# Kernel optimization log

Measured on AMD Instinct MI355X. Metric: run time of the kernel, lower is better.

## Reference

```python
import jax, jax.numpy as jnp
import numpy as np

B, C, H, W = 2, 192, 48, 512
EMB, HEADS, DOUT, MAXM, THR, EPS = 64, 2, 192, 64, 0.01, 1e-5
DV = DOUT // HEADS  # per-head value dim (96)


def setup_inputs() -> dict:
    key = jax.random.key(0)
    ks = jax.random.split(key, 16)
    s = 0.02
    inp = {
        "l": jax.random.normal(ks[0], (B, C, H, W), jnp.float32),
        "r": jax.random.normal(ks[1], (B, C, H, W), jnp.float32),
        "ln_l_g": jnp.ones((C,), jnp.float32),
        "ln_l_b": jnp.zeros((C,), jnp.float32),
        "ln_r_g": jnp.ones((C,), jnp.float32),
        "ln_r_b": jnp.zeros((C,), jnp.float32),
    }
    ki = 2
    for p in ("rtl", "ltr"):
        inp[p + "_wq"] = jax.random.normal(ks[ki], (HEADS * EMB, C, 3), jnp.float32) * s; ki += 1
        inp[p + "_bq"] = jnp.zeros((HEADS * EMB,), jnp.float32)
        inp[p + "_wk"] = jax.random.normal(ks[ki], (HEADS * EMB, C, 3), jnp.float32) * s; ki += 1
        inp[p + "_bk"] = jnp.zeros((HEADS * EMB,), jnp.float32)
        inp[p + "_wv"] = jax.random.normal(ks[ki], (DOUT, C, 3), jnp.float32) * s; ki += 1
        inp[p + "_bv"] = jnp.zeros((DOUT,), jnp.float32)
        inp[p + "_wo"] = jax.random.normal(ks[ki], (DOUT, DOUT), jnp.float32) * s; ki += 1
        inp[p + "_bo"] = jnp.zeros((DOUT,), jnp.float32)
    inp["ffl_w"] = jax.random.normal(ks[ki], (DOUT, DOUT), jnp.float32) * s; ki += 1
    inp["ffl_b"] = jnp.zeros((DOUT,), jnp.float32)
    inp["ffr_w"] = jax.random.normal(ks[ki], (DOUT, DOUT), jnp.float32) * s; ki += 1
    inp["ffr_b"] = jnp.zeros((DOUT,), jnp.float32)
    return inp


def _layernorm(x, g, b):
    m = x.mean(-1, keepdims=True)
    v = x.var(-1, keepdims=True)
    return (x - m) / jnp.sqrt(v + EPS) * g + b


def _conv1d(x, w, b):
    # x: [N, Cin, L], w: [Cout, Cin, 3], same padding
    y = jax.lax.conv_general_dilated(x, w, (1,), [(1, 1)], dimension_numbers=("NCH", "OIH", "NCH"))
    return y + b[None, :, None]


def _conv_attn(q_seq, k_seq, v_seq, wq, bq, wk, bk, wv, bv, wo, bo, mask):
    # q_seq/k_seq/v_seq: [N, L, C]; mask: [L, L] bool (True = masked)
    N, L, _ = q_seq.shape
    Q = _conv1d(q_seq.transpose(0, 2, 1), wq, bq).reshape(N, HEADS, EMB, L).transpose(0, 1, 3, 2)  # b h l d
    K = _conv1d(k_seq.transpose(0, 2, 1), wk, bk).reshape(N, HEADS, EMB, L).transpose(0, 1, 3, 2)
    V = _conv1d(v_seq.transpose(0, 2, 1), wv, bv).reshape(N, HEADS, DV, L).transpose(0, 1, 3, 2)
    A = jnp.einsum("bhqd,bhkd->bhqk", Q, K) / np.sqrt(EMB).astype(np.float32)
    A = jnp.where(mask, -jnp.inf, A)
    A = jax.nn.softmax(A, axis=-1)
    A = A * (A > THR)  # valid_mask thresholding after softmax
    O = jnp.einsum("bhqk,bhkd->bhqd", A, V)
    O = O.transpose(0, 2, 1, 3).reshape(N, L, DOUT)
    return jnp.einsum("nld,od->nlo", O, wo) + bo, A


def reference(l, r, ln_l_g, ln_l_b, ln_r_g, ln_r_b,
              rtl_wq, rtl_bq, rtl_wk, rtl_bk, rtl_wv, rtl_bv, rtl_wo, rtl_bo,
              ltr_wq, ltr_bq, ltr_wk, ltr_bk, ltr_wv, ltr_bv, ltr_wo, ltr_bo,
              ffl_w, ffl_b, ffr_w, ffr_b):
    ls = l.transpose(0, 2, 3, 1).reshape(B * H, W, C)  # (b h) w c
    rs = r.transpose(0, 2, 3, 1).reshape(B * H, W, C)
    ln_ = _layernorm(ls, ln_l_g, ln_l_b)
    rn_ = _layernorm(rs, ln_r_g, ln_r_b)
    i = jnp.arange(W)[:, None]
    j = jnp.arange(W)[None, :]
    mask_left = (j < i) | (j - i > MAXM)   # left query i attends keys j in [i, i+MAXM]
    mask_right = (j > i) | (i - j > MAXM)  # right query i attends keys j in [i-MAXM, i]
    l_mha, A_rtl = _conv_attn(ln_, rn_, rs, rtl_wq, rtl_bq, rtl_wk, rtl_bk, rtl_wv, rtl_bv, rtl_wo, rtl_bo, mask_left)
    r_mha, A_ltr = _conv_attn(rn_, ln_, ls, ltr_wq, ltr_bq, ltr_wk, ltr_bk, ltr_wv, ltr_bv, ltr_wo, ltr_bo, mask_right)
    lo = ls + l_mha
    ro = rs + r_mha
    lo = lo + (jnp.einsum("nwc,oc->nwo", lo, ffl_w) + ffl_b)
    ro = ro + (jnp.einsum("nwc,oc->nwo", ro, ffr_w) + ffr_b)
    l_out = lo.reshape(B, H, W, C).transpose(0, 3, 1, 2)
    r_out = ro.reshape(B, H, W, C).transpose(0, 3, 1, 2)
    return (l_out, r_out, A_rtl, A_ltr)
```

## Files before the change

### kernel.cpp

```cpp
#include <hip/hip_runtime.h>
#include <cstddef>
#include <cstdint>

constexpr int kC = 192;
constexpr int kW = 512;
constexpr int kHH = 48;

typedef unsigned short u16;
typedef __attribute__((ext_vector_type(8))) short bf16x8;
typedef __attribute__((ext_vector_type(4))) float f32x4;
typedef __attribute__((ext_vector_type(4))) unsigned short us4;

__device__ inline u16 f2bf(float f) {
  union { float f; uint32_t u; } v; v.f = f;
  uint32_t r = v.u + 0x7FFF + ((v.u >> 16) & 1);
  return (u16)(r >> 16);
}
__device__ inline float bf2f(u16 u) {
  return __uint_as_float(((uint32_t)u) << 16);
}

__global__ void __launch_bounds__(256) prep_kernel(
    const float* __restrict__ xl, const float* __restrict__ xr,
    const float* __restrict__ gl, const float* __restrict__ bl,
    const float* __restrict__ gr, const float* __restrict__ br,
    u16* __restrict__ lnl, u16* __restrict__ lraw,
    u16* __restrict__ lnr, u16* __restrict__ rraw,
    const float* wq0, const float* wk0, const float* wv0,
    const float* wq1, const float* wk1, const float* wv1,
    const float* bq0, const float* bk0, const float* bv0,
    const float* bq1, const float* bk1, const float* bv1,
    const float* wo0, const float* wo1, const float* fw0, const float* fw1,
    u16* __restrict__ wall, u16* __restrict__ pfw, float* __restrict__ ball) {
  int bid = blockIdx.x;
  int tid = threadIdx.x;
  if (bid >= 1536) {
    int idx = (bid - 1536) * 256 + tid;
    if (idx < 516096) {
      int dir = idx / 258048, off = idx % 258048;
      const float* src; int soff;
      if (off < 73728) { src = dir ? wq1 : wq0; soff = off; }
      else if (off < 147456) { src = dir ? wk1 : wk0; soff = off - 73728; }
      else { src = dir ? wv1 : wv0; soff = off - 147456; }
      int o = soff / 576, k = soff % 576, t = k / 192, c = k % 192;
      wall[idx] = f2bf(src[((size_t)o * kC + c) * 3 + t]);
    } else if (idx < 516096 + 147456) {
      int i2 = idx - 516096;
      int mat = i2 / 36864, off = i2 % 36864;
      const float* src = mat == 0 ? wo0 : mat == 1 ? wo1 : mat == 2 ? fw0 : fw1;
      pfw[i2] = f2bf(src[off]);
    } else if (idx < 516096 + 147456 + 896) {
      int bi = idx - 516096 - 147456;
      int dir = bi / 448, boff = bi % 448;
      const float* s; int so;
      if (boff < 128) { s = dir ? bq1 : bq0; so = boff; }
      else if (boff < 256) { s = dir ? bk1 : bk0; so = boff - 128; }
      else { s = dir ? bv1 : bv0; so = boff - 256; }
      ball[bi] = s[so];
    }
    return;
  }
  int w0 = (bid & 7) * 64;
  int n = (bid >> 3) % 96;
  int side = bid / 768;
  const float* x = side ? xr : xl;
  const float* g = side ? gr : gl;
  const float* b = side ? br : bl;
  u16* lnout = side ? lnr : lnl;
  u16* rawout = side ? rraw : lraw;
  int bb = n / kHH, h = n % kHH;
  __shared__ float tile[64][193];
  __shared__ float red[8][64];
  __shared__ float mean_s[64], rstd_s[64];
  int lane = tid & 63, wv = tid >> 6;
  for (int c = wv; c < kC; c += 4)
    tile[lane][c] = x[(((size_t)bb * kC + c) * kHH + h) * kW + w0 + lane];
  __syncthreads();
  {
    int w = tid & 63, part = tid >> 6;
    float s = 0.f, s2 = 0.f;
    const float* row = &tile[w][0];
    for (int c = part * 48; c < part * 48 + 48; ++c) {
      float v = row[c];
      s += v; s2 += v * v;
    }
    red[part][w] = s;
    red[part + 4][w] = s2;
  }
  __syncthreads();
  if (tid < 64) {
    float s = red[0][tid] + red[1][tid] + red[2][tid] + red[3][tid];
    float s2 = red[4][tid] + red[5][tid] + red[6][tid] + red[7][tid];
    float m = s * (1.f / 192.f);
    float var = s2 * (1.f / 192.f) - m * m;
    mean_s[tid] = m;
    rstd_s[tid] = rsqrtf(var + 1e-5f);
  }
  __syncthreads();
  for (int u = tid; u < 64 * 48; u += 256) {
    int w = u / 48, c4 = (u % 48) * 4;
    float mm = mean_s[w], rs = rstd_s[w];
    us4 lp, rp;
#pragma unroll
    for (int j = 0; j < 4; ++j) {
      float raw = tile[w][c4 + j];
      rp[j] = f2bf(raw);
      lp[j] = f2bf((raw - mm) * rs * g[c4 + j] + b[c4 + j]);
    }
    size_t idx = ((size_t)n * kW + w0 + w) * kC + c4;
    *reinterpret_cast<us4*>(&lnout[idx]) = lp;
    *reinterpret_cast<us4*>(&rawout[idx]) = rp;
  }
}

template <int NF>
__device__ __forceinline__ void conv_core(
    const u16* __restrict__ in, const u16* __restrict__ w2,
    int n, int l0, u16* As, f32x4 (&acc)[4][NF]) {
  int tid = threadIdx.x;
  int wid = tid >> 6, lane = tid & 63;
  int wm = wid >> 1, wn = wid & 1;
  int lr = lane & 15, g = lane >> 4;
  for (int u = tid; u < 130 * 48; u += 256) {
    int row = u / 48, q = u % 48;
    int l = l0 - 1 + row;
    us4 v = {0, 0, 0, 0};
    if (l >= 0 && l < kW)
      v = *reinterpret_cast<const us4*>(in + ((size_t)n * kW + l) * kC + q * 4);
    *reinterpret_cast<us4*>(&As[row * 200 + q * 4]) = v;
  }
  __syncthreads();
  const u16* wbase = w2 + (size_t)(wn * NF * 16 + lr) * 576 + g * 8;
#pragma unroll
  for (int t = 0; t < 3; ++t) {
#pragma unroll
    for (int c0 = 0; c0 < 192; c0 += 64) {
#pragma unroll
      for (int ks = 0; ks < 2; ++ks) {
        bf16x8 a[4], b[NF];
#pragma unroll
        for (int mf = 0; mf < 4; ++mf)
          a[mf] = *reinterpret_cast<const bf16x8*>(
              &As[(wm * 64 + mf * 16 + lr + t) * 200 + c0 + ks * 32 + g * 8]);
#pragma unroll
        for (int nf = 0; nf < NF; ++nf)
          b[nf] = *reinterpret_cast<const bf16x8*>(
              wbase + (size_t)nf * 16 * 576 + t * 192 + c0 + ks * 32);
#pragma unroll
        for (int mf = 0; mf < 4; ++mf)
#pragma unroll
          for (int nf = 0; nf < NF; ++nf)
            acc[mf][nf] = __builtin_amdgcn_mfma_f32_16x16x32_bf16(a[mf], b[nf], acc[mf][nf], 0, 0, 0);
      }
    }
  }
}

__global__ void __launch_bounds__(256) conv_qk(
    const u16* __restrict__ lnl, const u16* __restrict__ lnr,
    const u16* __restrict__ wall, const float* __restrict__ ball,
    u16* __restrict__ Qbf, u16* __restrict__ Kbf, float* __restrict__ A0) {
  if (blockIdx.y == 4) {
    int fid = blockIdx.z * 4 + blockIdx.x;
    int base_row = fid * 256;
    f32x4 z4 = {0.f, 0.f, 0.f, 0.f};
    for (int u = threadIdx.x; u < 256 * 128; u += 256) {
      int lrow = u >> 7, c4 = u & 127;
      int rg = base_row + lrow;
      int nh = rg >> 9, i = rg & 511;
      int q0 = i & ~63;
      int w1 = q0 + 128 > 512 ? 512 : q0 + 128;
      int col = c4 * 4;
      if (col < q0 || col >= w1)
        __builtin_nontemporal_store(z4, reinterpret_cast<f32x4*>(
            A0 + (size_t)nh * 262144 + (size_t)i * 512 + col));
    }
    return;
  }
  int l0 = blockIdx.x * 128;
  int jid = blockIdx.y;
  int n = blockIdx.z;
  int dir = jid >> 1, which = jid & 1;
  const u16* in = which == 0 ? (dir ? lnr : lnl) : (dir ? lnl : lnr);
  const u16* w2 = wall + (size_t)dir * 258048 + which * 73728;
  const float* bias = ball + dir * 448 + which * 128;

  __shared__ __attribute__((aligned(16))) u16 As[130 * 200];
  f32x4 acc[4][4] = {};
  conv_core<4>(in, w2, n, l0, As, acc);

  int tid = threadIdx.x;
  int wid = tid >> 6, lane = tid & 63;
  int wm = wid >> 1, wn = wid & 1;
  int lr = lane & 15, g = lane >> 4;
  __syncthreads();
  u16* Ts = As;
#pragma unroll
  for (int nf = 0; nf < 4; ++nf) {
    int o = wn * 64 + nf * 16 + lr;
    float bsv = bias[o];
#pragma unroll
    for (int mf = 0; mf < 4; ++mf) {
      int lbase = wm * 64 + mf * 16 + g * 4;
#pragma unroll
      for (int rg = 0; rg < 4; ++rg)
        Ts[(lbase + rg) * 132 + o] = f2bf(acc[mf][nf][rg] + bsv);
    }
  }
  __syncthreads();
  u16* outp = (which == 0 ? Qbf : Kbf) + (size_t)dir * 6291456;
  for (int u = tid; u < 4096; u += 256) {
    int hh = u >> 11;
    int rem = u & 2047;
    int l = rem >> 4, q4 = (rem & 15) * 4;
    us4 v = *reinterpret_cast<const us4*>(&Ts[l * 132 + hh * 64 + q4]);
    *reinterpret_cast<us4*>(
        &outp[((size_t)(n * 2 + hh) * kW + l0 + l) * 64 + q4]) = v;
  }
}

__global__ void __launch_bounds__(256) conv_v(
    const u16* __restrict__ lraw, const u16* __restrict__ rraw,
    const u16* __restrict__ wall, const float* __restrict__ ball,
    u16* __restrict__ Vbf, float* __restrict__ A1) {
  if (blockIdx.y == 2) {
    int fid = blockIdx.z * 4 + blockIdx.x;
    int base_row = fid * 256;
    f32x4 z4 = {0.f, 0.f, 0.f, 0.f};
    for (int u = threadIdx.x; u < 256 * 128; u += 256) {
      int lrow = u >> 7, c4 = u & 127;
      int rg = base_row + lrow;
      int nh = rg >> 9, i = rg & 511;
      int q0 = i & ~63;
      int w0 = q0 >= 64 ? q0 - 64 : 0;
      int col = c4 * 4;
      if (col < w0 || col >= q0 + 64)
        __builtin_nontemporal_store(z4, reinterpret_cast<f32x4*>(
            A1 + (size_t)nh * 262144 + (size_t)i * 512 + col));
    }
    return;
  }
  int l0 = blockIdx.x * 128;
  int dir = blockIdx.y;
  int n = blockIdx.z;
  const u16* in = dir ? lraw : rraw;
  const u16* w2 = wall + (size_t)dir * 258048 + 147456;
  const float* bias = ball + dir * 448 + 256;

  __shared__ __attribute__((aligned(16))) u16 As[130 * 200];
  f32x4 acc[4][6] = {};
  conv_core<6>(in, w2, n, l0, As, acc);

  int tid = threadIdx.x;
  int wid = tid >> 6, lane = tid & 63;
  int wm = wid >> 1, wn = wid & 1;
  int lr = lane & 15, g = lane >> 4;
  u16* outp = Vbf + (size_t)dir * 9437184;
#pragma unroll
  for (int nf = 0; nf < 6; ++nf) {
    int e = nf * 16 + lr;
    float bsv = bias[wn * 96 + e];
#pragma unroll
    for (int mf = 0; mf < 4; ++mf) {
      int lb = l0 + wm * 64 + mf * 16 + g * 4;
      us4 p;
#pragma unroll
      for (int rg = 0; rg < 4; ++rg) p[rg] = f2bf(acc[mf][nf][rg] + bsv);
      *reinterpret_cast<us4*>(&outp[((size_t)(n * 2 + wn) * 96 + e) * kW + lb]) = p;
    }
  }
}

__global__ void __launch_bounds__(256) attn_mfma(
    const u16* __restrict__ Qbf, const u16* __restrict__ Kbf,
    const u16* __restrict__ Vbf, float* __restrict__ Abase,
    u16* __restrict__ Obf) {
  int qb = blockIdx.x;
  int nh = blockIdx.y;
  int dir = blockIdx.z;
  int q0 = qb * 64;
  int k_start = dir == 0 ? q0 : (q0 >= 64 ? q0 - 64 : 0);
  int k_end = dir == 0 ? (q0 + 128 <= kW ? q0 + 128 : kW) : q0 + 64;
  int kfr = (k_end - k_start) >> 4;
  const u16* Q = Qbf + ((size_t)dir * 192 + nh) * kW * 64;
  const u16* K = Kbf + ((size_t)dir * 192 + nh) * kW * 64;
  const u16* V = Vbf + ((size_t)dir * 192 + nh) * 96 * kW;
  float* Aout = Abase + (size_t)dir * 50331648 + (size_t)nh * kW * kW;
  u16* Obase = Obf + (size_t)dir * 9437184;

  __shared__ __attribute__((aligned(16))) u16 smem[22272];
  u16* Ks = smem;
  u16* Ps = smem;
  u16* Vt = smem + 9216;

  int tid = threadIdx.x;
  int wid = tid >> 6, lane = tid & 63;
  int lr = lane & 15, g = lane >> 4;

  for (int u = tid; u < 128 * 16; u += 256) {
    int row = u >> 4, c4 = (u & 15) * 4;
    *reinterpret_cast<us4*>(&Ks[row * 72 + c4]) =
        *reinterpret_cast<const us4*>(&K[(size_t)(k_start + row) * 64 + c4]);
  }
  for (int u = tid; u < 96 * 32; u += 256) {
    int row = u >> 5, c4 = (u & 31) * 4;
    *reinterpret_cast<us4*>(&Vt[row * 136 + c4]) =
        *reinterpret_cast<const us4*>(&V[(size_t)row * kW + k_start + c4]);
  }
  const u16* Qrow = Q + (size_t)(q0 + wid * 16 + lr) * 64 + g * 8;
  bf16x8 bq0 = *reinterpret_cast<const bf16x8*>(Qrow);
  bf16x8 bq1 = *reinterpret_cast<const bf16x8*>(Qrow + 32);
  __syncthreads();

  int lo_k = q0 + wid * 16 - (dir == 0 ? 0 : 64) - k_start;
  int hi_k = q0 + wid * 16 + 15 + (dir == 0 ? 64 : 0) - k_start;

  f32x4 sT[8];
#pragma unroll
  for (int kf = 0; kf < 8; ++kf) sT[kf] = f32x4{0.f, 0.f, 0.f, 0.f};
#pragma unroll
  for (int kf = 0; kf < 8; ++kf) {
    if (kf * 16 + 15 >= lo_k && kf * 16 <= hi_k) {
      bf16x8 ak0 = *reinterpret_cast<const bf16x8*>(&Ks[(kf * 16 + lr) * 72 + g * 8]);
      sT[kf] = __builtin_amdgcn_mfma_f32_16x16x32_bf16(ak0, bq0, sT[kf], 0, 0, 0);
      bf16x8 ak1 = *reinterpret_cast<const bf16x8*>(&Ks[(kf * 16 + lr) * 72 + 32 + g * 8]);
      sT[kf] = __builtin_amdgcn_mfma_f32_16x16x32_bf16(ak1, bq1, sT[kf], 0, 0, 0);
    }
  }

  int i = q0 + wid * 16 + lr;
  float mx = -INFINITY;
#pragma unroll
  for (int kf = 0; kf < 8; ++kf) {
#pragma unroll
    for (int r = 0; r < 4; ++r) {
      int jj = k_start + kf * 16 + g * 4 + r;
      bool valid = (jj < k_end) &&
                   (dir == 0 ? (jj >= i && jj - i <= 64) : (jj <= i && i - jj <= 64));
      float v = valid ? sT[kf][r] * 0.125f : -INFINITY;
      sT[kf][r] = v;
      mx = fmaxf(mx, v);
    }
  }
  mx = fmaxf(mx, __shfl_xor(mx, 16));
  mx = fmaxf(mx, __shfl_xor(mx, 32));
  float ssum = 0.f;
#pragma unroll
  for (int kf = 0; kf < 8; ++kf) {
#pragma unroll
    for (int r = 0; r < 4; ++r) {
      float e = __expf(sT[kf][r] - mx);
      sT[kf][r] = e;
      ssum += e;
    }
  }
  ssum += __shfl_xor(ssum, 16);
  ssum += __shfl_xor(ssum, 32);
  float inv = 1.f / ssum;

  __syncthreads();

  {
    float* arow = Aout + (size_t)i * kW + k_start;
#pragma unroll
    for (int kf = 0; kf < 8; ++kf) {
      f32x4 pv;
      us4 pb;
#pragma unroll
      for (int r = 0; r < 4; ++r) {
        float p = sT[kf][r] * inv;
        p = (p > 0.01f) ? p : 0.f;
        pv[r] = p;
        pb[r] = f2bf(p);
      }
      *reinterpret_cast<us4*>(&Ps[(wid * 16 + lr) * 136 + kf * 16 + g * 4]) = pb;
      if (kf < kfr)
        __builtin_nontemporal_store(pv, reinterpret_cast<f32x4*>(arow + kf * 16 + g * 4));
    }
  }
  __syncthreads();

  f32x4 oacc[6];
#pragma unroll
  for (int ef = 0; ef < 6; ++ef) oacc[ef] = f32x4{0.f, 0.f, 0.f, 0.f};
#pragma unroll
  for (int kc = 0; kc < 4; ++kc) {
    if (kc * 32 + 31 >= lo_k && kc * 32 <= hi_k) {
      bf16x8 ap = *reinterpret_cast<const bf16x8*>(&Ps[(wid * 16 + lr) * 136 + kc * 32 + g * 8]);
#pragma unroll
      for (int ef = 0; ef < 6; ++ef) {
        bf16x8 bv = *reinterpret_cast<const bf16x8*>(&Vt[(ef * 16 + lr) * 136 + kc * 32 + g * 8]);
        oacc[ef] = __builtin_amdgcn_mfma_f32_16x16x32_bf16(ap, bv, oacc[ef], 0, 0, 0);
      }
    }
  }
  __syncthreads();
  u16* Os2 = smem;
#pragma unroll
  for (int ef = 0; ef < 6; ++ef) {
    int e = ef * 16 + lr;
#pragma unroll
    for (int r = 0; r < 4; ++r)
      Os2[(wid * 16 + g * 4 + r) * 104 + e] = f2bf(oacc[ef][r]);
  }
  __syncthreads();
  int n_ = nh >> 1, h_ = nh & 1;
  for (int u = tid; u < 64 * 24; u += 256) {
    int q = u / 24, c4 = (u % 24) * 4;
    *reinterpret_cast<us4*>(&Obase[((size_t)n_ * kW + q0 + q) * kC + h_ * 96 + c4]) =
        *reinterpret_cast<const us4*>(&Os2[q * 104 + c4]);
  }
}

__global__ void __launch_bounds__(256) projff_mfma(
    const u16* __restrict__ pfw,
    const float* __restrict__ bo0, const float* __restrict__ bo1,
    const float* __restrict__ fb0, const float* __restrict__ fb1,
    const u16* __restrict__ Obf, const u16* __restrict__ lraw,
    const u16* __restrict__ rraw, float* __restrict__ outbase) {
  int l0 = blockIdx.x * 64;
  int z = blockIdx.y;
  int dir = z / 96, n = z % 96;
  const u16* wo2 = pfw + (dir ? 36864 : 0);
  const u16* fw2 = pfw + 73728 + (dir ? 36864 : 0);
  const float* bo_ = dir ? bo1 : bo0;
  const float* fb_ = dir ? fb1 : fb0;
  const u16* Osrc = Obf + (size_t)dir * 9437184;
  const u16* resbf = dir ? rraw : lraw;
  float* outb = outbase + (size_t)dir * 9437184;
  int bb = n / kHH, h = n % kHH;

  __shared__ __attribute__((aligned(16))) u16 Xs[64 * 200];
  __shared__ __attribute__((aligned(16))) u16 Rs[64 * 200];

  int tid = threadIdx.x;
  int wid = tid >> 6, lane = tid & 63;
  int wm = wid >> 1, wn = wid & 1;
  int lr = lane & 15, g = lane >> 4;

  for (int u = tid; u < 64 * 48; u += 256) {
    int row = u / 48, q = u % 48;
    size_t src = ((size_t)n * kW + l0 + row) * kC + q * 4;
    *reinterpret_cast<us4*>(&Xs[row * 200 + q * 4]) =
        *reinterpret_cast<const us4*>(&Osrc[src]);
    *reinterpret_cast<us4*>(&Rs[row * 200 + q * 4]) =
        *reinterpret_cast<const us4*>(&resbf[src]);
  }
  __syncthreads();

  const u16* wobase = wo2 + (size_t)(wn * 96 + lr) * kC + g * 8;
  const u16* fwbase = fw2 + (size_t)(wn * 96 + lr) * kC + g * 8;

  f32x4 accp[2][6] = {};
#pragma unroll
  for (int c0 = 0; c0 < 192; c0 += 64) {
#pragma unroll
    for (int ks = 0; ks < 2; ++ks) {
      bf16x8 a[2], b[6];
#pragma unroll
      for (int m2 = 0; m2 < 2; ++m2)
        a[m2] = *reinterpret_cast<const bf16x8*>(
            &Xs[(wm * 32 + m2 * 16 + lr) * 200 + c0 + ks * 32 + g * 8]);
#pragma unroll
      for (int nf = 0; nf < 6; ++nf)
        b[nf] = *reinterpret_cast<const bf16x8*>(
            wobase + (size_t)nf * 16 * kC + c0 + ks * 32);
#pragma unroll
      for (int m2 = 0; m2 < 2; ++m2)
#pragma unroll
        for (int nf = 0; nf < 6; ++nf)
          accp[m2][nf] = __builtin_amdgcn_mfma_f32_16x16x32_bf16(a[m2], b[nf], accp[m2][nf], 0, 0, 0);
    }
  }
  __syncthreads();
#pragma unroll
  for (int nf = 0; nf < 6; ++nf) {
    int o = wn * 96 + nf * 16 + lr;
    float bv = bo_[o];
#pragma unroll
    for (int m2 = 0; m2 < 2; ++m2) {
#pragma unroll
      for (int r = 0; r < 4; ++r) {
        int l = wm * 32 + m2 * 16 + g * 4 + r;
        float v = accp[m2][nf][r] + bv + bf2f(Rs[l * 200 + o]);
        accp[m2][nf][r] = v;
        Xs[l * 200 + o] = f2bf(v);
      }
    }
  }
  __syncthreads();

  f32x4 accf[2][6] = {};
#pragma unroll
  for (int c0 = 0; c0 < 192; c0 += 64) {
#pragma unroll
    for (int ks = 0; ks < 2; ++ks) {
      bf16x8 a[2], b[6];
#pragma unroll
      for (int m2 = 0; m2 < 2; ++m2)
        a[m2] = *reinterpret_cast<const bf16x8*>(
            &Xs[(wm * 32 + m2 * 16 + lr) * 200 + c0 + ks * 32 + g * 8]);
#pragma unroll
      for (int nf = 0; nf < 6; ++nf)
        b[nf] = *reinterpret_cast<const bf16x8*>(
            fwbase + (size_t)nf * 16 * kC + c0 + ks * 32);
#pragma unroll
      for (int m2 = 0; m2 < 2; ++m2)
#pragma unroll
        for (int nf = 0; nf < 6; ++nf)
          accf[m2][nf] = __builtin_amdgcn_mfma_f32_16x16x32_bf16(a[m2], b[nf], accf[m2][nf], 0, 0, 0);
    }
  }
#pragma unroll
  for (int nf = 0; nf < 6; ++nf) {
    int o = wn * 96 + nf * 16 + lr;
    float bv = fb_[o];
#pragma unroll
    for (int m2 = 0; m2 < 2; ++m2) {
      f32x4 ov;
#pragma unroll
      for (int r = 0; r < 4; ++r)
        ov[r] = accf[m2][nf][r] + bv + accp[m2][nf][r];
      int l = l0 + wm * 32 + m2 * 16 + g * 4;
      *reinterpret_cast<f32x4*>(&outb[(((size_t)bb * kC + o) * kHH + h) * kW + l]) = ov;
    }
  }
}

extern "C" void kernel_launch(void* const* d_in, const int* in_sizes, int n_in,
                              void* d_out, int out_size, void* d_ws, size_t ws_size,
                              hipStream_t stream) {
  const float* l = (const float*)d_in[0];
  const float* r = (const float*)d_in[1];
  float* out = (float*)d_out;
  float* ws = (float*)d_ws;

  u16* lnl_bf  = (u16*)(ws + 0);
  u16* lnr_bf  = (u16*)(ws + 4718592);
  u16* lraw_bf = (u16*)(ws + 9437184);
  u16* rraw_bf = (u16*)(ws + 14155776);
  u16* wall    = (u16*)(ws + 18874368);
  float* ball  = ws + 19136512;
  u16* Qbf     = (u16*)(ws + 19137536);
  u16* Kbf     = (u16*)(ws + 25428992);
  u16* Vbf     = (u16*)(ws + 31720448);
  u16* Obf     = (u16*)(ws + 41157632);
  u16* pfw     = (u16*)(ws + 50594816);

  float* A0 = out + (size_t)18874368;
  float* A1 = out + (size_t)69206016;

  int wp_items = 516096 + 147456 + 896;
  int wp_blocks = (wp_items + 255) / 256;
  prep_kernel<<<1536 + wp_blocks, 256, 0, stream>>>(
      l, r, (const float*)d_in[2], (const float*)d_in[3],
      (const float*)d_in[4], (const float*)d_in[5],
      lnl_bf, lraw_bf, lnr_bf, rraw_bf,
      (const float*)d_in[6], (const float*)d_in[8], (const float*)d_in[10],
      (const float*)d_in[14], (const float*)d_in[16], (const float*)d_in[18],
      (const float*)d_in[7], (const float*)d_in[9], (const float*)d_in[11],
      (const float*)d_in[15], (const float*)d_in[17], (const float*)d_in[19],
      (const float*)d_in[12], (const float*)d_in[20],
      (const float*)d_in[22], (const float*)d_in[24],
      wall, pfw, ball);

  conv_qk<<<dim3(4, 5, 96), 256, 0, stream>>>(
      lnl_bf, lnr_bf, wall, ball, Qbf, Kbf, A0);
  conv_v<<<dim3(4, 3, 96), 256, 0, stream>>>(
      lraw_bf, rraw_bf, wall, ball, Vbf, A1);

  attn_mfma<<<dim3(8, 192, 2), 256, 0, stream>>>(
      Qbf, Kbf, Vbf, A0, Obf);

  projff_mfma<<<dim3(8, 192), 256, 0, stream>>>(
      pfw, (const float*)d_in[13], (const float*)d_in[21],
      (const float*)d_in[23], (const float*)d_in[25],
      Obf, lraw_bf, rraw_bf, out);
}
```

Before: 355.9 us.

## Fuse attention with output projection and feed-forward into one kernel

Merges the attention kernel and the projection/FF kernel so each block computes both heads for a 64-row tile, keeps the concatenated head outputs in shared memory, and then applies the output projection, residual and FF in place. This removes the bf16 O round trip through global memory and one kernel launch. In exchange the grid halves, the heads are processed sequentially inside each block, and shared memory per block grows to about 70KB, which may lower occupancy.

```diff
diff --git a/kernel.cpp b/kernel.cpp
--- a/kernel.cpp
+++ b/kernel.cpp
@@ -271,183 +271,162 @@
   }
 }
 
-__global__ void __launch_bounds__(256) attn_mfma(
+__global__ void __launch_bounds__(256) attn_projff(
     const u16* __restrict__ Qbf, const u16* __restrict__ Kbf,
-    const u16* __restrict__ Vbf, float* __restrict__ Abase,
-    u16* __restrict__ Obf) {
+    const u16* __restrict__ Vbf, const u16* __restrict__ pfw,
+    const float* __restrict__ bo0, const float* __restrict__ bo1,
+    const float* __restrict__ fb0, const float* __restrict__ fb1,
+    const u16* __restrict__ lraw, const u16* __restrict__ rraw,
+    float* __restrict__ Abase, float* __restrict__ outbase) {
   int qb = blockIdx.x;
-  int nh = blockIdx.y;
+  int n = blockIdx.y;
   int dir = blockIdx.z;
   int q0 = qb * 64;
   int k_start = dir == 0 ? q0 : (q0 >= 64 ? q0 - 64 : 0);
   int k_end = dir == 0 ? (q0 + 128 <= kW ? q0 + 128 : kW) : q0 + 64;
   int kfr = (k_end - k_start) >> 4;
-  const u16* Q = Qbf + ((size_t)dir * 192 + nh) * kW * 64;
-  const u16* K = Kbf + ((size_t)dir * 192 + nh) * kW * 64;
-  const u16* V = Vbf + ((size_t)dir * 192 + nh) * 96 * kW;
-  float* Aout = Abase + (size_t)dir * 50331648 + (size_t)nh * kW * kW;
-  u16* Obase = Obf + (size_t)dir * 9437184;
-
-  __shared__ __attribute__((aligned(16))) u16 smem[22272];
+
+  __shared__ __attribute__((aligned(16))) u16 smem[35072];
   u16* Ks = smem;
   u16* Ps = smem;
   u16* Vt = smem + 9216;
+  u16* Rs = smem;
+  u16* Os = smem + 22272;
 
   int tid = threadIdx.x;
   int wid = tid >> 6, lane = tid & 63;
   int lr = lane & 15, g = lane >> 4;
 
-  for (int u = tid; u < 128 * 16; u += 256) {
-    int row = u >> 4, c4 = (u & 15) * 4;
-    *reinterpret_cast<us4*>(&Ks[row * 72 + c4]) =
-        *reinterpret_cast<const us4*>(&K[(size_t)(k_start + row) * 64 + c4]);
-  }
-  for (int u = tid; u < 96 * 32; u += 256) {
-    int row = u >> 5, c4 = (u & 31) * 4;
-    *reinterpret_cast<us4*>(&Vt[row * 136 + c4]) =
-        *reinterpret_cast<const us4*>(&V[(size_t)row * kW + k_start + c4]);
-  }
-  const u16* Qrow = Q + (size_t)(q0 + wid * 16 + lr) * 64 + g * 8;
-  bf16x8 bq0 = *reinterpret_cast<const bf16x8*>(Qrow);
-  bf16x8 bq1 = *reinterpret_cast<const bf16x8*>(Qrow + 32);
-  __syncthreads();
-
   int lo_k = q0 + wid * 16 - (dir == 0 ? 0 : 64) - k_start;
   int hi_k = q0 + wid * 16 + 15 + (dir == 0 ? 64 : 0) - k_start;
-
-  f32x4 sT[8];
-#pragma unroll
-  for (int kf = 0; kf < 8; ++kf) sT[kf] = f32x4{0.f, 0.f, 0.f, 0.f};
-#pragma unroll
-  for (int kf = 0; kf < 8; ++kf) {
-    if (kf * 16 + 15 >= lo_k && kf * 16 <= hi_k) {
-      bf16x8 ak0 = *reinterpret_cast<const bf16x8*>(&Ks[(kf * 16 + lr) * 72 + g * 8]);
-      sT[kf] = __builtin_amdgcn_mfma_f32_16x16x32_bf16(ak0, bq0, sT[kf], 0, 0, 0);
-      bf16x8 ak1 = *reinterpret_cast<const bf16x8*>(&Ks[(kf * 16 + lr) * 72 + 32 + g * 8]);
-      sT[kf] = __builtin_amdgcn_mfma_f32_16x16x32_bf16(ak1, bq1, sT[kf], 0, 0, 0);
-    }
-  }
-
   int i = q0 + wid * 16 + lr;
-  float mx = -INFINITY;
-#pragma unroll
-  for (int kf = 0; kf < 8; ++kf) {
-#pragma unroll
-    for (int r = 0; r < 4; ++r) {
-      int jj = k_start + kf * 16 + g * 4 + r;
-      bool valid = (jj < k_end) &&
-                   (dir == 0 ? (jj >= i && jj - i <= 64) : (jj <= i && i - jj <= 64));
-      float v = valid ? sT[kf][r] * 0.125f : -INFINITY;
-      sT[kf][r] = v;
-      mx = fmaxf(mx, v);
-    }
-  }
-  mx = fmaxf(mx, __shfl_xor(mx, 16));
-  mx = fmaxf(mx, __shfl_xor(mx, 32));
-  float ssum = 0.f;
-#pragma unroll
-  for (int kf = 0; kf < 8; ++kf) {
-#pragma unroll
-    for (int r = 0; r < 4; ++r) {
-      float e = __expf(sT[kf][r] - mx);
-      sT[kf][r] = e;
-      ssum += e;
-    }
-  }
-  ssum += __shfl_xor(ssum, 16);
-  ssum += __shfl_xor(ssum, 32);
-  float inv = 1.f / ssum;
-
-  __syncthreads();
-
-  {
-    float* arow = Aout + (size_t)i * kW + k_start;
+
+#pragma unroll
+  for (int h = 0; h < 2; ++h) {
+    int nh = n * 2 + h;
+    const u16* Q = Qbf + ((size_t)dir * 192 + nh) * kW * 64;
+    const u16* K = Kbf + ((size_t)dir * 192 + nh) * kW * 64;
+    const u16* V = Vbf + ((size_t)dir * 192 + nh) * 96 * kW;
+    float* Aout = Abase + (size_t)dir * 50331648 + (size_t)nh * 262144;
+
+    for (int u = tid; u < 128 * 16; u += 256) {
+      int row = u >> 4, c4 = (u & 15) * 4;
+      *reinterpret_cast<us4*>(&Ks[row * 72 + c4]) =
+          *reinterpret_cast<const us4*>(&K[(size_t)(k_start + row) * 64 + c4]);
+    }
+    for (int u = tid; u < 96 * 32; u += 256) {
+      int row = u >> 5, c4 = (u & 31) * 4;
+      *reinterpret_cast<us4*>(&Vt[row * 136 + c4]) =
+          *reinterpret_cast<const us4*>(&V[(size_t)row * kW + k_start + c4]);
+    }
+    const u16* Qrow = Q + (size_t)(q0 + wid * 16 + lr) * 64 + g * 8;
+    bf16x8 bq0 = *reinterpret_cast<const bf16x8*>(Qrow);
+    bf16x8 bq1 = *reinterpret_cast<const bf16x8*>(Qrow + 32);
+    __syncthreads();
+
+    f32x4 sT[8];
+#pragma unroll
+    for (int kf = 0; kf < 8; ++kf) sT[kf] = f32x4{0.f, 0.f, 0.f, 0.f};
 #pragma unroll
     for (int kf = 0; kf < 8; ++kf) {
-      f32x4 pv;
-      us4 pb;
+      if (kf * 16 + 15 >= lo_k && kf * 16 <= hi_k) {
+        bf16x8 ak0 = *reinterpret_cast<const bf16x8*>(&Ks[(kf * 16 + lr) * 72 + g * 8]);
+        sT[kf] = __builtin_amdgcn_mfma_f32_16x16x32_bf16(ak0, bq0, sT[kf], 0, 0, 0);
+        bf16x8 ak1 = *reinterpret_cast<const bf16x8*>(&Ks[(kf * 16 + lr) * 72 + 32 + g * 8]);
+        sT[kf] = __builtin_amdgcn_mfma_f32_16x16x32_bf16(ak1, bq1, sT[kf], 0, 0, 0);
+      }
+    }
+
+    float mx = -INFINITY;
+#pragma unroll
+    for (int kf = 0; kf < 8; ++kf) {
 #pragma unroll
       for (int r = 0; r < 4; ++r) {
-        float p = sT[kf][r] * inv;
-        p = (p > 0.01f) ? p : 0.f;
-        pv[r] = p;
-        pb[r] = f2bf(p);
-      }
-      *reinterpret_cast<us4*>(&Ps[(wid * 16 + lr) * 136 + kf * 16 + g * 4]) = pb;
-      if (kf < kfr)
-        __builtin_nontemporal_store(pv, reinterpret_cast<f32x4*>(arow + kf * 16 + g * 4));
-    }
-  }
-  __syncthreads();
-
-  f32x4 oacc[6];
-#pragma unroll
-  for (int ef = 0; ef < 6; ++ef) oacc[ef] = f32x4{0.f, 0.f, 0.f, 0.f};
-#pragma unroll
-  for (int kc = 0; kc < 4; ++kc) {
-    if (kc * 32 + 31 >= lo_k && kc * 32 <= hi_k) {
-      bf16x8 ap = *reinterpret_cast<const bf16x8*>(&Ps[(wid * 16 + lr) * 136 + kc * 32 + g * 8]);
-#pragma unroll
-      for (int ef = 0; ef < 6; ++ef) {
-        bf16x8 bv = *reinterpret_cast<const bf16x8*>(&Vt[(ef * 16 + lr) * 136 + kc * 32 + g * 8]);
-        oacc[ef] = __builtin_amdgcn_mfma_f32_16x16x32_bf16(ap, bv, oacc[ef], 0, 0, 0);
-      }
-    }
-  }
-  __syncthreads();
-  u16* Os2 = smem;
-#pragma unroll
-  for (int ef = 0; ef < 6; ++ef) {
-    int e = ef * 16 + lr;
-#pragma unroll
-    for (int r = 0; r < 4; ++r)
-      Os2[(wid * 16 + g * 4 + r) * 104 + e] = f2bf(oacc[ef][r]);
-  }
-  __syncthreads();
-  int n_ = nh >> 1, h_ = nh & 1;
-  for (int u = tid; u < 64 * 24; u += 256) {
-    int q = u / 24, c4 = (u % 24) * 4;
-    *reinterpret_cast<us4*>(&Obase[((size_t)n_ * kW + q0 + q) * kC + h_ * 96 + c4]) =
-        *reinterpret_cast<const us4*>(&Os2[q * 104 + c4]);
-  }
-}
-
-__global__ void __launch_bounds__(256) projff_mfma(
-    const u16* __restrict__ pfw,
-    const float* __restrict__ bo0, const float* __restrict__ bo1,
-    const float* __restrict__ fb0, const float* __restrict__ fb1,
-    const u16* __restrict__ Obf, const u16* __restrict__ lraw,
-    const u16* __restrict__ rraw, float* __restrict__ outbase) {
-  int l0 = blockIdx.x * 64;
-  int z = blockIdx.y;
-  int dir = z / 96, n = z % 96;
+        int jj = k_start + kf * 16 + g * 4 + r;
+        bool valid = (jj < k_end) &&
+                     (dir == 0 ? (jj >= i && jj - i <= 64) : (jj <= i && i - jj <= 64));
+        float v = valid ? sT[kf][r] * 0.125f : -INFINITY;
+        sT[kf][r] = v;
+        mx = fmaxf(mx, v);
+      }
+    }
+    mx = fmaxf(mx, __shfl_xor(mx, 16));
+    mx = fmaxf(mx, __shfl_xor(mx, 32));
+    float ssum = 0.f;
+#pragma unroll
+    for (int kf = 0; kf < 8; ++kf) {
+#pragma unroll
+      for (int r = 0; r < 4; ++r) {
+        float e = __expf(sT[kf][r] - mx);
+        sT[kf][r] = e;
+        ssum += e;
+      }
+    }
+    ssum += __shfl_xor(ssum, 16);
+    ssum += __shfl_xor(ssum, 32);
+    float inv = 1.f / ssum;
+
+    __syncthreads();
+
+    {
+      float* arow = Aout + (size_t)i * kW + k_start;
+#pragma unroll
+      for (int kf = 0; kf < 8; ++kf) {
+        f32x4 pv;
+        us4 pb;
+#pragma unroll
+        for (int r = 0; r < 4; ++r) {
+          float p = sT[kf][r] * inv;
+          p = (p > 0.01f) ? p : 0.f;
+          pv[r] = p;
+          pb[r] = f2bf(p);
+        }
+        *reinterpret_cast<us4*>(&Ps[(wid * 16 + lr) * 136 + kf * 16 + g * 4]) = pb;
+        if (kf < kfr)
+          __builtin_nontemporal_store(pv, reinterpret_cast<f32x4*>(arow + kf * 16 + g * 4));
+      }
+    }
+    __syncthreads();
+
+    f32x4 oacc[6];
+#pragma unroll
+    for (int ef = 0; ef < 6; ++ef) oacc[ef] = f32x4{0.f, 0.f, 0.f, 0.f};
+#pragma unroll
+    for (int kc = 0; kc < 4; ++kc) {
+      if (kc * 32 + 31 >= lo_k && kc * 32 <= hi_k) {
+        bf16x8 ap = *reinterpret_cast<const bf16x8*>(&Ps[(wid * 16 + lr) * 136 + kc * 32 + g * 8]);
+#pragma unroll
+        for (int ef = 0; ef < 6; ++ef) {
+          bf16x8 bv = *reinterpret_cast<const bf16x8*>(&Vt[(ef * 16 + lr) * 136 + kc * 32 + g * 8]);
+          oacc[ef] = __builtin_amdgcn_mfma_f32_16x16x32_bf16(ap, bv, oacc[ef], 0, 0, 0);
+        }
+      }
+    }
+#pragma unroll
+    for (int ef = 0; ef < 6; ++ef) {
+      int e = h * 96 + ef * 16 + lr;
+#pragma unroll
+      for (int r = 0; r < 4; ++r)
+        Os[(wid * 16 + g * 4 + r) * 200 + e] = f2bf(oacc[ef][r]);
+    }
+    __syncthreads();
+  }
+
+  const u16* resbf = dir ? rraw : lraw;
+  for (int u = tid; u < 64 * 48; u += 256) {
+    int row = u / 48, q = u % 48;
+    *reinterpret_cast<us4*>(&Rs[row * 200 + q * 4]) =
+        *reinterpret_cast<const us4*>(&resbf[((size_t)n * kW + q0 + row) * kC + q * 4]);
+  }
+
   const u16* wo2 = pfw + (dir ? 36864 : 0);
   const u16* fw2 = pfw + 73728 + (dir ? 36864 : 0);
   const float* bo_ = dir ? bo1 : bo0;
   const float* fb_ = dir ? fb1 : fb0;
-  const u16* Osrc = Obf + (size_t)dir * 9437184;
-  const u16* resbf = dir ? rraw : lraw;
   float* outb = outbase + (size_t)dir * 9437184;
-  int bb = n / kHH, h = n % kHH;
-
-  __shared__ __attribute__((aligned(16))) u16 Xs[64 * 200];
-  __shared__ __attribute__((aligned(16))) u16 Rs[64 * 200];
-
-  int tid = threadIdx.x;
-  int wid = tid >> 6, lane = tid & 63;
+  int bb = n / kHH, hh_ = n % kHH;
+
   int wm = wid >> 1, wn = wid & 1;
-  int lr = lane & 15, g = lane >> 4;
-
-  for (int u = tid; u < 64 * 48; u += 256) {
-    int row = u / 48, q = u % 48;
-    size_t src = ((size_t)n * kW + l0 + row) * kC + q * 4;
-    *reinterpret_cast<us4*>(&Xs[row * 200 + q * 4]) =
-        *reinterpret_cast<const us4*>(&Osrc[src]);
-    *reinterpret_cast<us4*>(&Rs[row * 200 + q * 4]) =
-        *reinterpret_cast<const us4*>(&resbf[src]);
-  }
-  __syncthreads();
-
   const u16* wobase = wo2 + (size_t)(wn * 96 + lr) * kC + g * 8;
   const u16* fwbase = fw2 + (size_t)(wn * 96 + lr) * kC + g * 8;
 
@@ -460,7 +439,7 @@
 #pragma unroll
       for (int m2 = 0; m2 < 2; ++m2)
         a[m2] = *reinterpret_cast<const bf16x8*>(
-            &Xs[(wm * 32 + m2 * 16 + lr) * 200 + c0 + ks * 32 + g * 8]);
+            &Os[(wm * 32 + m2 * 16 + lr) * 200 + c0 + ks * 32 + g * 8]);
 #pragma unroll
       for (int nf = 0; nf < 6; ++nf)
         b[nf] = *reinterpret_cast<const bf16x8*>(
@@ -484,7 +463,7 @@
         int l = wm * 32 + m2 * 16 + g * 4 + r;
         float v = accp[m2][nf][r] + bv + bf2f(Rs[l * 200 + o]);
         accp[m2][nf][r] = v;
-        Xs[l * 200 + o] = f2bf(v);
+        Os[l * 200 + o] = f2bf(v);
       }
     }
   }
@@ -499,7 +478,7 @@
 #pragma unroll
       for (int m2 = 0; m2 < 2; ++m2)
         a[m2] = *reinterpret_cast<const bf16x8*>(
-            &Xs[(wm * 32 + m2 * 16 + lr) * 200 + c0 + ks * 32 + g * 8]);
+            &Os[(wm * 32 + m2 * 16 + lr) * 200 + c0 + ks * 32 + g * 8]);
 #pragma unroll
       for (int nf = 0; nf < 6; ++nf)
         b[nf] = *reinterpret_cast<const bf16x8*>(
@@ -521,8 +500,8 @@
 #pragma unroll
       for (int r = 0; r < 4; ++r)
         ov[r] = accf[m2][nf][r] + bv + accp[m2][nf][r];
-      int l = l0 + wm * 32 + m2 * 16 + g * 4;
-      *reinterpret_cast<f32x4*>(&outb[(((size_t)bb * kC + o) * kHH + h) * kW + l]) = ov;
+      int l = q0 + wm * 32 + m2 * 16 + g * 4;
+      *reinterpret_cast<f32x4*>(&outb[(((size_t)bb * kC + o) * kHH + hh_) * kW + l]) = ov;
     }
   }
 }
@@ -544,7 +523,6 @@
   u16* Qbf     = (u16*)(ws + 19137536);
   u16* Kbf     = (u16*)(ws + 25428992);
   u16* Vbf     = (u16*)(ws + 31720448);
-  u16* Obf     = (u16*)(ws + 41157632);
   u16* pfw     = (u16*)(ws + 50594816);
 
   float* A0 = out + (size_t)18874368;
@@ -569,11 +547,9 @@
   conv_v<<<dim3(4, 3, 96), 256, 0, stream>>>(
       lraw_bf, rraw_bf, wall, ball, Vbf, A1);
 
-  attn_mfma<<<dim3(8, 192, 2), 256, 0, stream>>>(
-      Qbf, Kbf, Vbf, A0, Obf);
-
-  projff_mfma<<<dim3(8, 192), 256, 0, stream>>>(
-      pfw, (const float*)d_in[13], (const float*)d_in[21],
+  attn_projff<<<dim3(8, 96, 2), 256, 0, stream>>>(
+      Qbf, Kbf, Vbf, pfw,
+      (const float*)d_in[13], (const float*)d_in[21],
       (const float*)d_in[23], (const float*)d_in[25],
-      Obf, lraw_bf, rraw_bf, out);
-}
+      lraw_bf, rraw_bf, A0, out);
+}
```

New measurement: 348.3 us (median of 3 runs). 2.1% less time.
